# Performance work log

Hardware: AMD Instinct MI355X
Metric: run time of the kernel (lower is better)

## Reference

```python
import jax, jax.numpy as jnp
import numpy as np
import math

B, S, DIM = 2, 2048, 2048
H, HD, RD = 16, 128, 64
LKV, LQ = 512, 1536

def _rope(x, cos, sin):
    # x: (B,S,H,RD); interpret consecutive pairs as complex, multiply by e^{i theta}
    b, s, h, d = x.shape
    xr = x.reshape(b, s, h, d // 2, 2)
    xre, xim = xr[..., 0], xr[..., 1]
    c = cos[None, :, None, :]  # (1,S,1,d/2)
    sn = sin[None, :, None, :]
    ore = xre * c - xim * sn
    oim = xre * sn + xim * c
    return jnp.stack([ore, oim], axis=-1).reshape(b, s, h, d)

def setup_inputs() -> dict:
    key = jax.random.key(0)
    ks = jax.random.split(key, 12)
    def w(k, shape, fan_in):
        return jax.random.normal(k, shape, jnp.float32) * (1.0 / math.sqrt(fan_in))
    x = jax.random.normal(ks[0], (B, S, DIM), jnp.float32)
    # RoPE tables for decoupled rotary subspace of width RD
    inv_freq = 1.0 / (10000.0 ** (np.arange(0, RD, 2, dtype=np.float32) / RD))
    ang = np.outer(np.arange(S, dtype=np.float32), inv_freq)  # (S, RD/2)
    freq_cos = jnp.asarray(np.cos(ang), jnp.float32)
    freq_sin = jnp.asarray(np.sin(ang), jnp.float32)
    return {
        "x": x, "freq_cos": freq_cos, "freq_sin": freq_sin,
        "Wkv": w(ks[1], (DIM, LKV), DIM),          # latent_kv (no bias)
        "Wlq": w(ks[2], (DIM, LQ), DIM),           # latent_q (no bias)
        "Wq": w(ks[3], (LQ, H * HD), LQ),          # query (no bias)
        "Wk": w(ks[4], (LKV, H * HD), LKV),        # key (no bias)
        "Wv": w(ks[5], (LKV, H * HD), LKV),        # value (no bias)
        "Wqr": w(ks[6], (LQ, H * RD), LQ),         # decop_rot_q (bias=True)
        "bqr": jnp.zeros((H * RD,), jnp.float32),
        "Wkr": w(ks[7], (DIM, H * RD), DIM),       # decop_rot_k (bias=True)
        "bkr": jnp.zeros((H * RD,), jnp.float32),
        "Wo": w(ks[8], (H * HD, DIM), H * HD),     # out_proj (bias=True)
        "bo": jnp.zeros((DIM,), jnp.float32),
    }

def reference(x, freq_cos, freq_sin, Wkv, Wlq, Wq, Wk, Wv, Wqr, bqr, Wkr, bkr, Wo, bo):
    b, s, _ = x.shape
    cq = x @ Wlq                      # (B,S,LQ)
    ckv = x @ Wkv                     # (B,S,LKV)
    q = (cq @ Wq).reshape(b, s, H, HD)
    qr = _rope((cq @ Wqr + bqr).reshape(b, s, H, RD), freq_cos, freq_sin)
    k = (ckv @ Wk).reshape(b, s, H, HD)
    kr = _rope((x @ Wkr + bkr).reshape(b, s, H, RD), freq_cos, freq_sin)
    v = (ckv @ Wv).reshape(b, s, H, HD)
    qf = jnp.concatenate([q, qr], axis=-1)   # (B,S,H,HD+RD)
    kf = jnp.concatenate([k, kr], axis=-1)
    scale = 1.0 / math.sqrt(HD + RD)
    scores = jnp.einsum('bqhd,bkhd->bhqk', qf, kf) * scale
    # masked=True path: causal tril mask over full seq_len
    mask = jnp.tril(jnp.ones((s, s), bool))
    scores = jnp.where(mask[None, None], scores, -jnp.inf)
    att = jax.nn.softmax(scores.astype(jnp.float32), axis=-1).astype(qf.dtype)
    out = jnp.einsum('bhqk,bkhd->bqhd', att, v).reshape(b, s, H * HD)
    return out @ Wo + bo
```

## Files before the change

### kernel.cpp

```cpp
#include <hip/hip_runtime.h>
#include <hip/hip_bf16.h>
#include <stdint.h>

#define S_LEN 2048
#define NB 2
#define NH 16
#define HDIM 128
#define RDIM 64
#define DF 192
#define MROWS 4096

typedef __bf16 bf16_t;
typedef __attribute__((ext_vector_type(8))) __bf16 bf16x8;
typedef __attribute__((ext_vector_type(4))) __bf16 bf16x4;
typedef __attribute__((ext_vector_type(4))) float f32x4;
typedef __attribute__((ext_vector_type(4))) float float4v;

__device__ __forceinline__ void gload_lds16(const bf16_t* g, bf16_t* l) {
  __builtin_amdgcn_global_load_lds(
      (const __attribute__((address_space(1))) void*)g,
      (__attribute__((address_space(3))) void*)l, 16, 0, 0);
}

__global__ __launch_bounds__(256) void convert_bf16(const float* __restrict__ in,
                                                    bf16_t* __restrict__ out, int n4) {
  int i = blockIdx.x * 256 + threadIdx.x;
  if (i >= n4) return;
  float4v v = *reinterpret_cast<const float4v*>(&in[(size_t)i * 4]);
  bf16x4 o;
  o[0] = (bf16_t)v[0]; o[1] = (bf16_t)v[1]; o[2] = (bf16_t)v[2]; o[3] = (bf16_t)v[3];
  *reinterpret_cast<bf16x4*>(&out[(size_t)i * 4]) = o;
}

struct TrDesc { const float* src; bf16_t* dst; int K; int N; int nbx; int base; };
struct TrPack { TrDesc d[8]; };

__global__ __launch_bounds__(256) void transpose_all(TrPack p) {
  __shared__ float t[64][65];
  const int bid = blockIdx.x;
  int m = 0;
#pragma unroll
  for (int i = 1; i < 8; ++i) m += (bid >= p.d[i].base);
  const TrDesc td = p.d[m];
  const int local = bid - td.base;
  const int n0 = (local % td.nbx) * 64, k0 = (local / td.nbx) * 64;
  const int tx = threadIdx.x & 63, ty = threadIdx.x >> 6;
#pragma unroll
  for (int i = ty; i < 64; i += 4)
    t[i][tx] = td.src[(size_t)(k0 + i) * td.N + n0 + tx];
  __syncthreads();
#pragma unroll
  for (int i = ty; i < 64; i += 4)
    td.dst[(size_t)(n0 + i) * td.K + k0 + tx] = (bf16_t)t[tx][i];
}

struct EpiParams {
  bf16_t* o0;
  bf16_t* o1;
  bf16_t* o2;
  float* outf;
  const float* bias;
  const float* cosb;
  const float* sinb;
};

template <int MODE>
__device__ __forceinline__ void gemm_body(const bf16_t* __restrict__ A,
                                          const bf16_t* __restrict__ Bt,
                                          int N, int K, int m0, int n0,
                                          bf16_t* As, bf16_t* Bs, EpiParams ep) {
  const int tid = threadIdx.x;
  const int lane = tid & 63, w = tid >> 6;
  const int l15 = lane & 15, lg = lane >> 4;
  const int mw = (w >> 1) * 64, nw = (w & 1) * 64;

  f32x4 acc[4][4] = {};
  const int row_ld = tid >> 2;
  const int col8 = (tid & 3) * 8;
  const bf16_t* ag = A + (size_t)(m0 + row_ld) * K + col8;
  const bf16_t* bg = Bt + (size_t)(n0 + row_ld) * K + col8;
  const unsigned wbase = (unsigned)(tid & ~63u) * 8;

  for (int k0 = 0; k0 < K; k0 += 32) {
    __syncthreads();
    gload_lds16(ag + k0, As + wbase);
    gload_lds16(ag + (size_t)64 * K + k0, As + 2048 + wbase);
    gload_lds16(bg + k0, Bs + wbase);
    gload_lds16(bg + (size_t)64 * K + k0, Bs + 2048 + wbase);
    __syncthreads();
    bf16x8 a[4], b[4];
#pragma unroll
    for (int i = 0; i < 4; ++i)
      a[i] = *reinterpret_cast<const bf16x8*>(&As[(mw + i * 16 + l15) * 32 + lg * 8]);
#pragma unroll
    for (int i = 0; i < 4; ++i)
      b[i] = *reinterpret_cast<const bf16x8*>(&Bs[(nw + i * 16 + l15) * 32 + lg * 8]);
#pragma unroll
    for (int i = 0; i < 4; ++i)
#pragma unroll
      for (int j = 0; j < 4; ++j)
        acc[i][j] = __builtin_amdgcn_mfma_f32_16x16x32_bf16(a[i], b[j], acc[i][j], 0, 0, 0);
  }

#pragma unroll
  for (int i = 0; i < 4; ++i)
#pragma unroll
    for (int j = 0; j < 4; ++j) {
      const int col = n0 + nw + j * 16 + l15;
#pragma unroll
      for (int r = 0; r < 4; ++r) {
        const int row = m0 + mw + i * 16 + lg * 4 + r;
        float v = acc[i][j][r];
        const int b = row >> 11, s = row & 2047;
        if constexpr (MODE == 1) {
          ep.outf[(size_t)row * N + col] = v + ep.bias[col];
        } else if constexpr (MODE == 5) {
          if (col < 1536) {
            ep.o0[(size_t)row * 1536 + col] = (bf16_t)v;
          } else if (col < 2048) {
            ep.o1[(size_t)row * 512 + (col - 1536)] = (bf16_t)v;
          } else {
            const int c2 = col - 2048;
            float vb = v + ep.bias[c2];
            float other = __shfl_xor(vb, 1, 64);
            const int h = c2 >> 6, dr = c2 & 63;
            const int fi = dr >> 1;
            const float c = ep.cosb[s * 32 + fi];
            const float sn = ep.sinb[s * 32 + fi];
            const float o = (c2 & 1) ? (other * sn + vb * c) : (vb * c - other * sn);
            ep.o2[(((size_t)(b * NH + h)) * S_LEN + s) * DF + 128 + dr] = (bf16_t)o;
          }
        } else if constexpr (MODE == 6) {
          if (col < 2048) {
            const int h = col >> 7, d = col & 127;
            ep.o0[(((size_t)(b * NH + h)) * S_LEN + s) * DF + d] = (bf16_t)v;
          } else {
            const int c2 = col - 2048;
            float vb = v + ep.bias[c2];
            float other = __shfl_xor(vb, 1, 64);
            const int h = c2 >> 6, dr = c2 & 63;
            const int fi = dr >> 1;
            const float c = ep.cosb[s * 32 + fi];
            const float sn = ep.sinb[s * 32 + fi];
            const float o = (c2 & 1) ? (other * sn + vb * c) : (vb * c - other * sn);
            ep.o0[(((size_t)(b * NH + h)) * S_LEN + s) * DF + 128 + dr] = (bf16_t)o;
          }
        } else {
          if (col < 2048) {
            const int h = col >> 7, d = col & 127;
            ep.o0[(((size_t)(b * NH + h)) * S_LEN + s) * DF + d] = (bf16_t)v;
          } else {
            const int c2 = col - 2048;
            const int h = c2 >> 7, d = c2 & 127;
            ep.o1[(((size_t)(b * NH + h)) * HDIM + d) * S_LEN + s] = (bf16_t)v;
          }
        }
      }
    }
}

template <int MODE>
__global__ __launch_bounds__(256) void gemm_bt(const bf16_t* __restrict__ A,
                                               const bf16_t* __restrict__ Bt,
                                               int N, int K, EpiParams ep) {
  __shared__ alignas(16) bf16_t As[128 * 32];
  __shared__ alignas(16) bf16_t Bs[128 * 32];
  const int gx = gridDim.x;
  const int nwg = gx * gridDim.y;
  int flat = blockIdx.y * gx + blockIdx.x;
  flat = (flat & 7) * (nwg >> 3) + (flat >> 3);
  const int m0 = (flat / gx) * 128, n0 = (flat % gx) * 128;
  gemm_body<MODE>(A, Bt, N, K, m0, n0, As, Bs, ep);
}

__global__ __launch_bounds__(256) void gemm_bt67(const bf16_t* __restrict__ A6,
                                                 const bf16_t* __restrict__ Bt6,
                                                 const bf16_t* __restrict__ A7,
                                                 const bf16_t* __restrict__ Bt7,
                                                 EpiParams ep6, EpiParams ep7) {
  __shared__ alignas(16) bf16_t As[128 * 32];
  __shared__ alignas(16) bf16_t Bs[128 * 32];
  const int bid = blockIdx.x;
  if (bid < 768) {
    int flat = (bid & 7) * 96 + (bid >> 3);
    const int m0 = (flat / 24) * 128, n0 = (flat % 24) * 128;
    gemm_body<6>(A6, Bt6, 3072, 1536, m0, n0, As, Bs, ep6);
  } else {
    int b2 = bid - 768;
    int flat = (b2 & 7) * 128 + (b2 >> 3);
    const int m0 = (flat / 32) * 128, n0 = (flat % 32) * 128;
    gemm_body<7>(A7, Bt7, 4096, 512, m0, n0, As, Bs, ep7);
  }
}

__global__ __launch_bounds__(256, 2) void attn_fwd(const bf16_t* __restrict__ qf,
                                                   const bf16_t* __restrict__ kf,
                                                   const bf16_t* __restrict__ vT,
                                                   bf16_t* __restrict__ att) {
  const int tid = threadIdx.x;
  const int lane = tid & 63, w = tid >> 6;
  const int l15 = lane & 15, lg = lane >> 4;
  const int l = blockIdx.x;
  const int bh = (l & 7) * 4 + ((l >> 3) & 3);
  const int qchunk = l >> 5;
  const int qb0 = (15 - qchunk) * 128;
  const int q0 = qb0 + w * 32;
  const float scale = 0.07216878364870322f;

  __shared__ alignas(16) bf16_t Ks[64 * 192];
  __shared__ alignas(16) bf16_t Vs[128 * 64];
  __shared__ alignas(16) bf16_t Ps[4 * 2048];

  bf16x8 qfr[2][6];
#pragma unroll
  for (int mf = 0; mf < 2; ++mf) {
    const bf16_t* qptr = qf + ((size_t)bh * S_LEN + q0 + mf * 16 + l15) * DF + lg * 8;
#pragma unroll
    for (int d = 0; d < 6; ++d)
      qfr[mf][d] = *reinterpret_cast<const bf16x8*>(qptr + d * 32);
  }

  f32x4 o[2][8] = {};
  float mrun[2] = {-1e30f, -1e30f}, lsum[2] = {0.0f, 0.0f};

  const bf16_t* kb0 = kf + (size_t)bh * S_LEN * DF;
  const bf16_t* vb0 = vT + (size_t)bh * HDIM * S_LEN;
  const int njt = qb0 / 64 + 2;
  const int wslot = tid & ~63;

  for (int jt = 0; jt < njt; ++jt) {
    const int j0 = jt * 64;
    __syncthreads();
    const bf16_t* kTile = kb0 + (size_t)j0 * DF;
#pragma unroll
    for (int i = 0; i < 6; ++i) {
      const int s = i * 256 + tid;
      const int row = s / 24;
      const int c = s - row * 24;
      const int cs = c ^ (row & 7);
      gload_lds16(kTile + (size_t)row * DF + cs * 8,
                  Ks + (size_t)(i * 256 + wslot) * 8);
    }
    const bf16_t* vTile = vb0 + j0;
#pragma unroll
    for (int i = 0; i < 4; ++i) {
      const int s = i * 256 + tid;
      const int row = s >> 3;
      const int c = s & 7;
      const int cs = c ^ (row & 7);
      gload_lds16(vTile + (size_t)row * S_LEN + cs * 8,
                  Vs + (size_t)(i * 256 + wslot) * 8);
    }
    __syncthreads();

    if (j0 > q0 + 31) continue;

    f32x4 sa[2][4] = {};
    __builtin_amdgcn_s_setprio(1);
#pragma unroll
    for (int jf = 0; jf < 4; ++jf) {
      const int krow = jf * 16 + l15;
      const int ksw = krow & 7;
#pragma unroll
      for (int d = 0; d < 6; ++d) {
        const int kc = (4 * d + lg) ^ ksw;
        bf16x8 kfr = *reinterpret_cast<const bf16x8*>(&Ks[krow * 192 + kc * 8]);
#pragma unroll
        for (int mf = 0; mf < 2; ++mf)
          sa[mf][jf] =
              __builtin_amdgcn_mfma_f32_16x16x32_bf16(kfr, qfr[mf][d], sa[mf][jf], 0, 0, 0);
      }
    }
    __builtin_amdgcn_s_setprio(0);

#pragma unroll
    for (int mf = 0; mf < 2; ++mf) {
      const int qi = q0 + mf * 16 + l15;
      const bool full = (j0 + 63 <= q0 + mf * 16);
      float sv[16];
#pragma unroll
      for (int jf = 0; jf < 4; ++jf)
#pragma unroll
        for (int r = 0; r < 4; ++r) {
          float x = sa[mf][jf][r] * scale;
          if (!full) {
            const int j = j0 + jf * 16 + lg * 4 + r;
            if (j > qi) x = -1e30f;
          }
          sv[jf * 4 + r] = x;
        }

      float a8[8];
#pragma unroll
      for (int i = 0; i < 8; ++i) a8[i] = fmaxf(sv[i], sv[i + 8]);
#pragma unroll
      for (int i = 0; i < 4; ++i) a8[i] = fmaxf(a8[i], a8[i + 4]);
      float mx = fmaxf(fmaxf(a8[0], a8[1]), fmaxf(a8[2], a8[3]));
      mx = fmaxf(mx, __shfl_xor(mx, 16, 64));
      mx = fmaxf(mx, __shfl_xor(mx, 32, 64));

      if (__any(mx > mrun[mf] + 8.0f)) {
        const float mn = fmaxf(mrun[mf], mx);
        const float alpha = __expf(mrun[mf] - mn);
        mrun[mf] = mn;
        lsum[mf] *= alpha;
        float af[4];
#pragma unroll
        for (int r = 0; r < 4; ++r) af[r] = __shfl(alpha, lg * 4 + r, 16);
#pragma unroll
        for (int dt = 0; dt < 8; ++dt)
#pragma unroll
          for (int r = 0; r < 4; ++r) o[mf][dt][r] *= af[r];
      }

#pragma unroll
      for (int i = 0; i < 16; ++i) sv[i] = __expf(sv[i] - mrun[mf]);
      float s8[8];
#pragma unroll
      for (int i = 0; i < 8; ++i) s8[i] = sv[i] + sv[i + 8];
#pragma unroll
      for (int i = 0; i < 4; ++i) s8[i] = s8[i] + s8[i + 4];
      float sm = (s8[0] + s8[1]) + (s8[2] + s8[3]);
      sm += __shfl_xor(sm, 16, 64);
      sm += __shfl_xor(sm, 32, 64);
      lsum[mf] += sm;

#pragma unroll
      for (int jf = 0; jf < 4; ++jf) {
        bf16x4 pk;
#pragma unroll
        for (int r = 0; r < 4; ++r) pk[r] = (bf16_t)sv[jf * 4 + r];
        const int key = jf * 16 + lg * 4;
        *reinterpret_cast<bf16x4*>(
            &Ps[w * 2048 + mf * 1024 + l15 * 64 + (key ^ ((l15 & 7) << 3))]) = pk;
      }
    }
    asm volatile("s_waitcnt lgkmcnt(0)" ::: "memory");
    __builtin_amdgcn_sched_barrier(0);
    bf16x8 pfr[2][2];
#pragma unroll
    for (int mf = 0; mf < 2; ++mf)
#pragma unroll
      for (int jk = 0; jk < 2; ++jk)
        pfr[mf][jk] = *reinterpret_cast<const bf16x8*>(
            &Ps[w * 2048 + mf * 1024 + l15 * 64 + (((jk * 4 + lg) ^ (l15 & 7)) << 3)]);

    __builtin_amdgcn_s_setprio(1);
#pragma unroll
    for (int dt = 0; dt < 8; ++dt) {
      const int vrow = dt * 16 + l15;
      const int vsw = vrow & 7;
#pragma unroll
      for (int jk = 0; jk < 2; ++jk) {
        const int vc = (jk * 4 + lg) ^ vsw;
        bf16x8 vfr = *reinterpret_cast<const bf16x8*>(&Vs[vrow * 64 + vc * 8]);
#pragma unroll
        for (int mf = 0; mf < 2; ++mf)
          o[mf][dt] =
              __builtin_amdgcn_mfma_f32_16x16x32_bf16(pfr[mf][jk], vfr, o[mf][dt], 0, 0, 0);
      }
    }
    __builtin_amdgcn_s_setprio(0);
  }

  const int b = bh >> 4, h = bh & 15;
#pragma unroll
  for (int mf = 0; mf < 2; ++mf) {
    const float inv = 1.0f / lsum[mf];
    float iv[4];
#pragma unroll
    for (int r = 0; r < 4; ++r) iv[r] = __shfl(inv, lg * 4 + r, 16);
#pragma unroll
    for (int dt = 0; dt < 8; ++dt)
#pragma unroll
      for (int r = 0; r < 4; ++r) {
        const int s = q0 + mf * 16 + lg * 4 + r;
        att[((size_t)b * S_LEN + s) * 2048 + h * 128 + dt * 16 + l15] =
            (bf16_t)(o[mf][dt][r] * iv[r]);
      }
  }
}

extern "C" void kernel_launch(void* const* d_in, const int* in_sizes, int n_in,
                              void* d_out, int out_size, void* d_ws, size_t ws_size,
                              hipStream_t stream) {
  const float* x    = (const float*)d_in[0];
  const float* fcos = (const float*)d_in[1];
  const float* fsin = (const float*)d_in[2];
  const float* Wkv  = (const float*)d_in[3];
  const float* Wlq  = (const float*)d_in[4];
  const float* Wq   = (const float*)d_in[5];
  const float* Wk   = (const float*)d_in[6];
  const float* Wv   = (const float*)d_in[7];
  const float* Wqr  = (const float*)d_in[8];
  const float* bqr  = (const float*)d_in[9];
  const float* Wkr  = (const float*)d_in[10];
  const float* bkr  = (const float*)d_in[11];
  const float* Wo   = (const float*)d_in[12];
  const float* bo   = (const float*)d_in[13];
  float* out = (float*)d_out;

  char* ws = (char*)d_ws;
  size_t off = 0;
  auto alloc = [&](size_t bytes) {
    void* p = ws + off;
    off += (bytes + 255) & ~(size_t)255;
    return p;
  };
  bf16_t* xb    = (bf16_t*)alloc((size_t)MROWS * 2048 * 2);
  bf16_t* WcatA = (bf16_t*)alloc((size_t)3072 * 2048 * 2);
  bf16_t* WcatB = (bf16_t*)alloc((size_t)3072 * 1536 * 2);
  bf16_t* WcatC = (bf16_t*)alloc((size_t)4096 * 512 * 2);
  bf16_t* WoT   = (bf16_t*)alloc((size_t)2048 * 2048 * 2);
  bf16_t* cq    = (bf16_t*)alloc((size_t)MROWS * 1536 * 2);
  bf16_t* ckv   = (bf16_t*)alloc((size_t)MROWS * 512 * 2);
  bf16_t* qfb   = (bf16_t*)alloc((size_t)NB * NH * S_LEN * DF * 2);
  bf16_t* kfb   = (bf16_t*)alloc((size_t)NB * NH * S_LEN * DF * 2);
  bf16_t* vTb   = (bf16_t*)alloc((size_t)NB * NH * HDIM * S_LEN * 2);
  bf16_t* attb  = (bf16_t*)alloc((size_t)MROWS * 2048 * 2);

  {
    int n4 = (MROWS * 2048) / 4;
    convert_bf16<<<dim3((n4 + 255) / 256), dim3(256), 0, stream>>>(x, xb, n4);
  }
  {
    TrPack p;
    int base = 0;
    auto set = [&](int i, const float* s, bf16_t* d, int K, int N) {
      p.d[i] = {s, d, K, N, N / 64, base};
      base += (N / 64) * (K / 64);
    };
    set(0, Wlq, WcatA, 2048, 1536);
    set(1, Wkv, WcatA + (size_t)1536 * 2048, 2048, 512);
    set(2, Wkr, WcatA + (size_t)2048 * 2048, 2048, 1024);
    set(3, Wq,  WcatB, 1536, 2048);
    set(4, Wqr, WcatB + (size_t)2048 * 1536, 1536, 1024);
    set(5, Wk,  WcatC, 512, 2048);
    set(6, Wv,  WcatC + (size_t)2048 * 512, 512, 2048);
    set(7, Wo,  WoT, 2048, 2048);
    transpose_all<<<dim3(base), dim3(256), 0, stream>>>(p);
  }

  EpiParams ep{}, ep2{};

  ep = {cq, ckv, kfb, nullptr, bkr, fcos, fsin};
  gemm_bt<5><<<dim3(3072 / 128, MROWS / 128), dim3(256), 0, stream>>>(
      xb, WcatA, 3072, 2048, ep);
  ep  = {qfb, nullptr, nullptr, nullptr, bqr, fcos, fsin};
  ep2 = {kfb, vTb, nullptr, nullptr, nullptr, nullptr, nullptr};
  gemm_bt67<<<dim3(1792), dim3(256), 0, stream>>>(cq, WcatB, ckv, WcatC, ep, ep2);
  attn_fwd<<<dim3(512), dim3(256), 0, stream>>>(qfb, kfb, vTb, attb);
  ep = {nullptr, nullptr, nullptr, out, bo, nullptr, nullptr};
  gemm_bt<1><<<dim3(2048 / 128, MROWS / 128), dim3(256), 0, stream>>>(
      attb, WoT, 2048, 2048, ep);
}
```

Baseline: 364.9 us.

## Rewrite projection GEMMs with 256x128 tiles and a triple-buffered swizzled LDS pipeline

Replaces the 128x128, K=32, single-buffer GEMM with a 512-thread (8-wave) kernel using 256x128 tiles and K=64 steps. Tiles are staged through a 3-deep LDS ring with direct global-to-LDS loads, waited on with explicit vmcnt counts, so global loads overlap MFMA work instead of waiting at two barriers per step. LDS columns are XOR-swizzled to reduce bank conflicts, and s_setprio raises priority around the MFMA section. The cost is about 144 KB of LDS per block, which limits each CU to one block, and fewer, larger workgroups that may leave the last wave of the grid less evenly balanced.

```diff
diff --git a/kernel.cpp b/kernel.cpp
--- a/kernel.cpp
+++ b/kernel.cpp
@@ -65,41 +65,72 @@
 };
 
 template <int MODE>
-__device__ __forceinline__ void gemm_body(const bf16_t* __restrict__ A,
-                                          const bf16_t* __restrict__ Bt,
-                                          int N, int K, int m0, int n0,
-                                          bf16_t* As, bf16_t* Bs, EpiParams ep) {
+__device__ __forceinline__ void gemm8p_body(const bf16_t* __restrict__ A,
+                                            const bf16_t* __restrict__ Bt,
+                                            int N, int K, int m0, int n0,
+                                            bf16_t (*Ab)[256 * 64],
+                                            bf16_t (*Bb)[128 * 64], EpiParams ep) {
   const int tid = threadIdx.x;
   const int lane = tid & 63, w = tid >> 6;
   const int l15 = lane & 15, lg = lane >> 4;
   const int mw = (w >> 1) * 64, nw = (w & 1) * 64;
+  const int nt = K >> 6;
+
+  auto stage = [&](int t, int buf) {
+    const int k0 = t << 6;
+#pragma unroll
+    for (int j = 0; j < 4; ++j) {
+      const int s = j * 512 + tid;
+      const int row = s >> 3, c = s & 7;
+      const int cs = c ^ (row & 7);
+      gload_lds16(A + (size_t)(m0 + row) * K + k0 + cs * 8, &Ab[buf][s * 8]);
+    }
+#pragma unroll
+    for (int j = 0; j < 2; ++j) {
+      const int s = j * 512 + tid;
+      const int row = s >> 3, c = s & 7;
+      const int cs = c ^ (row & 7);
+      gload_lds16(Bt + (size_t)(n0 + row) * K + k0 + cs * 8, &Bb[buf][s * 8]);
+    }
+  };
 
   f32x4 acc[4][4] = {};
-  const int row_ld = tid >> 2;
-  const int col8 = (tid & 3) * 8;
-  const bf16_t* ag = A + (size_t)(m0 + row_ld) * K + col8;
-  const bf16_t* bg = Bt + (size_t)(n0 + row_ld) * K + col8;
-  const unsigned wbase = (unsigned)(tid & ~63u) * 8;
-
-  for (int k0 = 0; k0 < K; k0 += 32) {
-    __syncthreads();
-    gload_lds16(ag + k0, As + wbase);
-    gload_lds16(ag + (size_t)64 * K + k0, As + 2048 + wbase);
-    gload_lds16(bg + k0, Bs + wbase);
-    gload_lds16(bg + (size_t)64 * K + k0, Bs + 2048 + wbase);
-    __syncthreads();
-    bf16x8 a[4], b[4];
-#pragma unroll
-    for (int i = 0; i < 4; ++i)
-      a[i] = *reinterpret_cast<const bf16x8*>(&As[(mw + i * 16 + l15) * 32 + lg * 8]);
-#pragma unroll
-    for (int i = 0; i < 4; ++i)
-      b[i] = *reinterpret_cast<const bf16x8*>(&Bs[(nw + i * 16 + l15) * 32 + lg * 8]);
-#pragma unroll
-    for (int i = 0; i < 4; ++i)
-#pragma unroll
-      for (int j = 0; j < 4; ++j)
-        acc[i][j] = __builtin_amdgcn_mfma_f32_16x16x32_bf16(a[i], b[j], acc[i][j], 0, 0, 0);
+  stage(0, 0);
+  stage(1, 1);
+
+  for (int t = 0; t < nt; ++t) {
+    const int cur = t % 3;
+    if (t + 1 < nt) {
+      asm volatile("s_waitcnt vmcnt(6)" ::: "memory");
+    } else {
+      asm volatile("s_waitcnt vmcnt(0)" ::: "memory");
+    }
+    __builtin_amdgcn_s_barrier();
+    __builtin_amdgcn_sched_barrier(0);
+    if (t + 2 < nt) stage(t + 2, (t + 2) % 3);
+
+    __builtin_amdgcn_s_setprio(1);
+#pragma unroll
+    for (int kk = 0; kk < 2; ++kk) {
+      const int c = kk * 4 + lg;
+      bf16x8 a[4], b[4];
+#pragma unroll
+      for (int i = 0; i < 4; ++i) {
+        const int r = mw + i * 16 + l15;
+        a[i] = *reinterpret_cast<const bf16x8*>(&Ab[cur][r * 64 + ((c ^ (r & 7)) << 3)]);
+      }
+#pragma unroll
+      for (int j = 0; j < 4; ++j) {
+        const int r = nw + j * 16 + l15;
+        b[j] = *reinterpret_cast<const bf16x8*>(&Bb[cur][r * 64 + ((c ^ (r & 7)) << 3)]);
+      }
+#pragma unroll
+      for (int i = 0; i < 4; ++i)
+#pragma unroll
+        for (int j = 0; j < 4; ++j)
+          acc[i][j] = __builtin_amdgcn_mfma_f32_16x16x32_bf16(a[i], b[j], acc[i][j], 0, 0, 0);
+    }
+    __builtin_amdgcn_s_setprio(0);
   }
 
 #pragma unroll
@@ -160,36 +191,36 @@
 }
 
 template <int MODE>
-__global__ __launch_bounds__(256) void gemm_bt(const bf16_t* __restrict__ A,
-                                               const bf16_t* __restrict__ Bt,
-                                               int N, int K, EpiParams ep) {
-  __shared__ alignas(16) bf16_t As[128 * 32];
-  __shared__ alignas(16) bf16_t Bs[128 * 32];
-  const int gx = gridDim.x;
-  const int nwg = gx * gridDim.y;
-  int flat = blockIdx.y * gx + blockIdx.x;
-  flat = (flat & 7) * (nwg >> 3) + (flat >> 3);
-  const int m0 = (flat / gx) * 128, n0 = (flat % gx) * 128;
-  gemm_body<MODE>(A, Bt, N, K, m0, n0, As, Bs, ep);
-}
-
-__global__ __launch_bounds__(256) void gemm_bt67(const bf16_t* __restrict__ A6,
-                                                 const bf16_t* __restrict__ Bt6,
-                                                 const bf16_t* __restrict__ A7,
-                                                 const bf16_t* __restrict__ Bt7,
-                                                 EpiParams ep6, EpiParams ep7) {
-  __shared__ alignas(16) bf16_t As[128 * 32];
-  __shared__ alignas(16) bf16_t Bs[128 * 32];
+__global__ __launch_bounds__(512, 2) void gemm8p(const bf16_t* __restrict__ A,
+                                                 const bf16_t* __restrict__ Bt,
+                                                 int N, int K, EpiParams ep) {
+  __shared__ alignas(16) bf16_t Ab[3][256 * 64];
+  __shared__ alignas(16) bf16_t Bb[3][128 * 64];
+  const int nwg = gridDim.x;
+  int f = blockIdx.x;
+  f = (f & 7) * (nwg >> 3) + (f >> 3);
+  const int nbx = N >> 7;
+  const int m0 = (f / nbx) * 256, n0 = (f % nbx) * 128;
+  gemm8p_body<MODE>(A, Bt, N, K, m0, n0, Ab, Bb, ep);
+}
+
+__global__ __launch_bounds__(512, 2) void gemm8p67(const bf16_t* __restrict__ A6,
+                                                   const bf16_t* __restrict__ Bt6,
+                                                   const bf16_t* __restrict__ A7,
+                                                   const bf16_t* __restrict__ Bt7,
+                                                   EpiParams ep6, EpiParams ep7) {
+  __shared__ alignas(16) bf16_t Ab[3][256 * 64];
+  __shared__ alignas(16) bf16_t Bb[3][128 * 64];
   const int bid = blockIdx.x;
-  if (bid < 768) {
-    int flat = (bid & 7) * 96 + (bid >> 3);
-    const int m0 = (flat / 24) * 128, n0 = (flat % 24) * 128;
-    gemm_body<6>(A6, Bt6, 3072, 1536, m0, n0, As, Bs, ep6);
+  if (bid < 384) {
+    int f = (bid & 7) * 48 + (bid >> 3);
+    const int m0 = (f / 24) * 256, n0 = (f % 24) * 128;
+    gemm8p_body<6>(A6, Bt6, 3072, 1536, m0, n0, Ab, Bb, ep6);
   } else {
-    int b2 = bid - 768;
-    int flat = (b2 & 7) * 128 + (b2 >> 3);
-    const int m0 = (flat / 32) * 128, n0 = (flat % 32) * 128;
-    gemm_body<7>(A7, Bt7, 4096, 512, m0, n0, As, Bs, ep7);
+    int b2 = bid - 384;
+    int f = (b2 & 7) * 64 + (b2 >> 3);
+    const int m0 = (f / 32) * 256, n0 = (f % 32) * 128;
+    gemm8p_body<7>(A7, Bt7, 4096, 512, m0, n0, Ab, Bb, ep7);
   }
 }
 
@@ -444,13 +475,11 @@
   EpiParams ep{}, ep2{};
 
   ep = {cq, ckv, kfb, nullptr, bkr, fcos, fsin};
-  gemm_bt<5><<<dim3(3072 / 128, MROWS / 128), dim3(256), 0, stream>>>(
-      xb, WcatA, 3072, 2048, ep);
+  gemm8p<5><<<dim3(384), dim3(512), 0, stream>>>(xb, WcatA, 3072, 2048, ep);
   ep  = {qfb, nullptr, nullptr, nullptr, bqr, fcos, fsin};
   ep2 = {kfb, vTb, nullptr, nullptr, nullptr, nullptr, nullptr};
-  gemm_bt67<<<dim3(1792), dim3(256), 0, stream>>>(cq, WcatB, ckv, WcatC, ep, ep2);
+  gemm8p67<<<dim3(896), dim3(512), 0, stream>>>(cq, WcatB, ckv, WcatC, ep, ep2);
   attn_fwd<<<dim3(512), dim3(256), 0, stream>>>(qfb, kfb, vTb, attb);
   ep = {nullptr, nullptr, nullptr, out, bo, nullptr, nullptr};
-  gemm_bt<1><<<dim3(2048 / 128, MROWS / 128), dim3(256), 0, stream>>>(
-      attb, WoT, 2048, 2048, ep);
-}
+  gemm8p<1><<<dim3(256), dim3(512), 0, stream>>>(attb, WoT, 2048, 2048, ep);
+}
```

After: 382.2 us. 1.05x slower.
